# Performance work log

Hardware: AMD Instinct MI355X
Metric: run time of the kernel (lower is better)

Reference implementation:

```python
import jax, jax.numpy as jnp
import numpy as np
from math import factorial

# ---- static sizes from S2ConvNet_original ----
B_IN, B1, B2 = 30, 10, 6   # bandwidths: input S2 grid, after conv1 (SO3), after conv2 (SO3)
F1, F2, FOUT = 20, 40, 10
BATCH = 128


def _wigner_d(l, beta):
    """Wigner small-d matrix d^l_{m',m}(beta); rows m'=-l..l, cols m=-l..l."""
    cb, sb = np.cos(beta / 2.0), np.sin(beta / 2.0)
    d = np.zeros((2 * l + 1, 2 * l + 1))
    for i, mp in enumerate(range(-l, l + 1)):
        for j, m in enumerate(range(-l, l + 1)):
            pref = np.sqrt(float(factorial(l + mp) * factorial(l - mp) * factorial(l + m) * factorial(l - m)))
            acc = 0.0
            for s in range(max(0, m - mp), min(l + m, l - mp) + 1):
                den = factorial(l + m - s) * factorial(s) * factorial(mp - m + s) * factorial(l - mp - s)
                acc += ((-1.0) ** (mp - m + s) / den) * cb ** (2 * l + m - mp - 2 * s) * sb ** (mp - m + 2 * s)
            d[i, j] = pref * acc
    return d


def _dh_quad(b):
    """Driscoll-Healy beta grid / weights: sum_j w_j g(beta_j) ~ int_0^pi g(b) sin(b) db."""
    j = np.arange(2 * b)
    beta = np.pi * (2 * j + 1) / (4 * b)
    k = np.arange(b)[:, None]
    w = (2.0 / b) * np.sin(beta) * np.sum(np.sin((2 * k + 1) * beta[None, :]) / (2 * k + 1), axis=0)
    return beta, w


def _s2_grid(max_beta=np.pi / 8, n_alpha=8, n_beta=3):
    beta = np.arange(1, n_beta + 1) * max_beta / n_beta
    alpha = np.linspace(0, 2 * np.pi, n_alpha, endpoint=False)
    Bm, Am = np.meshgrid(beta, alpha, indexing='ij')
    return np.stack([Bm.ravel(), Am.ravel()], 1)  # [24, 2]


def _so3_grid(max_beta=np.pi / 8, max_gamma=2 * np.pi, n_alpha=8, n_beta=3, n_gamma=8):
    beta = np.arange(1, n_beta + 1) * max_beta / n_beta
    alpha = np.linspace(0, 2 * np.pi, n_alpha, endpoint=False)
    pre_gamma = np.linspace(0, max_gamma, n_gamma, endpoint=False)
    Bm, Am, Cm = np.meshgrid(beta, alpha, pre_gamma, indexing='ij')
    return np.stack([Bm.ravel(), Am.ravel(), (Cm - Am).ravel()], 1)  # [192, 3]


# ---------- conv1: S2 analysis (b 30 -> 10) ----------
_beta30, _qw30 = _dh_quad(B_IN)
_A1 = np.concatenate(
    [np.stack([_wigner_d(l, bb)[:, l] for bb in _beta30])  # d^l_{m,0}(beta_j): [60, 2l+1]
     * (_qw30 * (2 * np.pi / (2 * B_IN)))[:, None]
     for l in range(B1)], axis=1)  # [60, 100]
_A1J = jnp.asarray(_A1.astype(np.float32))
_M1 = np.concatenate([np.arange(-l, l + 1) for l in range(B1)])
_M1_IDX = np.mod(_M1, 2 * B_IN)

_g1 = _s2_grid()
_Y1 = np.concatenate(
    [np.stack([_wigner_d(l, bb)[:, l] for bb in _g1[:, 0]])
     * np.exp(-1j * np.outer(_g1[:, 1], np.arange(-l, l + 1)))
     for l in range(B1)], axis=1)  # [24, 100] complex
_Y1J = jnp.asarray(_Y1.astype(np.complex64))
_SC1 = float(1.0 / np.sqrt(len(_g1) * 1 * (B1 ** 4) / (B_IN ** 2)))

# ---------- SO3 synthesis tables at b=10 ----------
_beta10, _qw10 = _dh_quad(B1)
_D1S = [jnp.asarray(((2 * l + 1) * np.stack([_wigner_d(l, bb) for bb in _beta10])).astype(np.float32)) for l in range(B1)]
_FM1 = [np.mod(np.arange(-l, l + 1), 2 * B1) for l in range(B1)]

# ---------- conv2: SO3 analysis (b 10 -> 6) ----------
_W3 = np.concatenate(
    [(np.stack([_wigner_d(l, bb) for bb in _beta10])  # [20, 2l+1, 2l+1]
      * (_qw10 * (2 * np.pi / (2 * B1)) ** 2)[:, None, None]).reshape(2 * B1, -1)
     for l in range(B2)], axis=1)  # [20, 286]
_W3J = jnp.asarray(_W3.astype(np.float32))
_M2 = np.concatenate([np.repeat(np.arange(-l, l + 1), 2 * l + 1) for l in range(B2)])
_N2 = np.concatenate([np.tile(np.arange(-l, l + 1), 2 * l + 1) for l in range(B2)])
_M2_IDX = np.mod(_M2, 2 * B1)
_N2_IDX = np.mod(_N2, 2 * B1)

_g2 = _so3_grid()
_Y2 = np.concatenate(
    [np.stack([_wigner_d(l, bb) for bb in _g2[:, 0]]).reshape(len(_g2), -1)
     * (np.exp(-1j * np.outer(_g2[:, 1], np.arange(-l, l + 1)))[:, :, None]
        * np.exp(-1j * np.outer(_g2[:, 2], np.arange(-l, l + 1)))[:, None, :]).reshape(len(_g2), -1)
     for l in range(B2)], axis=1)  # [192, 286] complex: D^l_{mn}(alpha,beta,gamma)
_Y2J = jnp.asarray(_Y2.astype(np.complex64))
_SC2 = float(1.0 / np.sqrt(len(_g2) * F1 * (B2 ** 3) / (B1 ** 3)))

# ---------- SO3 synthesis tables at b=6 + integration weights ----------
_beta6, _qw6 = _dh_quad(B2)
_D2S = [jnp.asarray(((2 * l + 1) * np.stack([_wigner_d(l, bb) for bb in _beta6])).astype(np.float32)) for l in range(B2)]
_FM2 = [np.mod(np.arange(-l, l + 1), 2 * B2) for l in range(B2)]
_W_INT = jnp.asarray((_qw6 * (2 * np.pi / (2 * B2)) ** 2).astype(np.float32))


def _forward(x, k1, bias1, k2, bias2, w_out, b_lin):
    Bn = x.shape[0]
    # ===== conv1: S2 correlation -> function on SO(3) at b=10 =====
    xf = jnp.fft.fft(x.astype(jnp.complex64), axis=-1)                 # FFT over alpha: [B,1,60,60]
    xhat = jnp.einsum('bfjs,js->sbf', xf[..., _M1_IDX], _A1J)          # [100,B,1] S2 spectrum
    k1h = jnp.einsum('iop,ps->sio', (k1 * _SC1).astype(jnp.complex64), _Y1J)  # [100,1,F1]
    Ffreq = jnp.zeros((Bn, F1, 2 * B1, 2 * B1, 2 * B1), jnp.complex64)  # [B,F1,beta,m,n]
    for l in range(B1):
        s0, s1 = l * l, (l + 1) * (l + 1)
        # z^l_{mn} = sum_fin xhat^l_m conj(khat^l_n)  (outer product per degree l)
        zl = jnp.einsum('mbi,nio->bmno', xhat[s0:s1], jnp.conj(k1h[s0:s1]))
        fb = jnp.einsum('bmno,jmn->bojmn', zl, _D1S[l])                # (2l+1) d^l_{mn}(beta_j)
        Ffreq = Ffreq.at[:, :, :, _FM1[l][:, None], _FM1[l][None, :]].add(fb)
    x1 = jnp.fft.ifft2(Ffreq, axes=(-2, -1)).real * float((2 * B1) ** 2)  # synth over alpha,gamma
    x1 = jax.nn.relu(x1 + bias1[None, :, None, None, None])            # [B,F1,20,20,20]
    # ===== conv2: SO(3) correlation -> b=6 =====
    x1f = jnp.fft.fft2(x1.astype(jnp.complex64), axes=(-2, -1))        # FFT over alpha,gamma
    xhat2 = jnp.einsum('bfjs,js->sbf', x1f[:, :, :, _M2_IDX, _N2_IDX], _W3J)  # [286,B,F1]
    k2h = jnp.einsum('iop,ps->sio', (k2 * _SC2).astype(jnp.complex64), _Y2J)  # [286,F1,F2]
    Ffreq2 = jnp.zeros((Bn, F2, 2 * B2, 2 * B2, 2 * B2), jnp.complex64)
    base = 0
    for l in range(B2):
        L = 2 * l + 1
        xl = xhat2[base:base + L * L].reshape(L, L, Bn, F1)            # [m,k,B,Fin]
        gl = jnp.conj(k2h[base:base + L * L].reshape(L, L, F1, F2))    # [n,k,Fin,Fout]
        zl = jnp.einsum('mkbi,nkio->bmno', xl, gl)                     # z^l = xhat^l ghat^l^H
        fb = jnp.einsum('bmno,jmn->bojmn', zl, _D2S[l])
        Ffreq2 = Ffreq2.at[:, :, :, _FM2[l][:, None], _FM2[l][None, :]].add(fb)
        base += L * L
    x2 = jnp.fft.ifft2(Ffreq2, axes=(-2, -1)).real * float((2 * B2) ** 2)
    x2 = jax.nn.relu(x2 + bias2[None, :, None, None, None])            # [B,F2,12,12,12]
    # ===== so3_integrate + linear head =====
    feat = jnp.einsum('bfjkp,j->bf', x2, _W_INT)                       # [B,F2]
    return feat @ w_out.T + b_lin


def setup_inputs() -> dict:
    key = jax.random.key(0)
    ks = jax.random.split(key, 4)
    return {
        'x': jax.random.normal(ks[0], (BATCH, 1, 2 * B_IN, 2 * B_IN), jnp.float32),
        'k1': jax.random.normal(ks[1], (1, F1, len(_g1)), jnp.float32),
        'bias1': jnp.zeros((F1,), jnp.float32),
        'k2': jax.random.normal(ks[2], (F1, F2, len(_g2)), jnp.float32),
        'bias2': jnp.zeros((F2,), jnp.float32),
        'w_out': jax.random.normal(ks[3], (FOUT, F2), jnp.float32) / np.sqrt(F2).astype(np.float32),
        'b_lin': jnp.zeros((FOUT,), jnp.float32),
    }


def reference(x, k1, bias1, k2, bias2, w_out, b_lin):
    return _forward(x, k1, bias1, k2, bias2, w_out, b_lin)
```

## Files before the change

### kernel.cpp

```cpp
#include <hip/hip_runtime.h>
#include <math.h>

#define PI_D 3.14159265358979323846

#define BATCH 128
#define F1 20
#define F2 40
#define FOUT 10
#define NS1 100
#define NS2 286
#define NH2 146

typedef float v2f __attribute__((ext_vector_type(2)));
#define PKFMA(a,b,c) __builtin_elementwise_fma((a),(b),(c))
#define SW(v) __builtin_shufflevector((v),(v),1,0)
static __device__ __forceinline__ v2f bc2(float s){ return (v2f){s,s}; }
static __device__ __forceinline__ v2f ldv(const float2* p){ return *(const v2f*)p; }

#define GLOAD_LDS16(g,l) __builtin_amdgcn_global_load_lds( \
  (const __attribute__((address_space(1))) void*)(g), \
  (__attribute__((address_space(3))) void*)(l), 16, 0, 0)

__constant__ int ZB10c[11] = {0,1,10,35,84,165,286,455,680,969,1330};
__constant__ int B2OFFc[7] = {0,1,10,35,84,165,286};
__constant__ int HOFFc[7]  = {0,1,6,19,44,85,146};
__constant__ float2 E8c[8] = {
  { 1.f, 0.f}, { 0.70710678118654752f,-0.70710678118654752f},
  { 0.f,-1.f}, {-0.70710678118654752f,-0.70710678118654752f},
  {-1.f, 0.f}, {-0.70710678118654752f, 0.70710678118654752f},
  { 0.f, 1.f}, { 0.70710678118654752f, 0.70710678118654752f}};

#define WFENCE do{ __builtin_amdgcn_sched_barrier(0); \
  asm volatile("s_waitcnt lgkmcnt(0)" ::: "memory"); \
  __builtin_amdgcn_sched_barrier(0); }while(0)

__device__ inline void h_decode(int h, int& l, int& m, int& n){
  l=0; while(HOFFc[l+1]<=h) ++l;
  int r=h-HOFFc[l], L=2*l+1;
  if(r<l+1){ n=0; m=r; }
  else { int q=r-(l+1); n=q/L+1; m=q%L-l; }
}

__device__ inline double ipow_d(double x, int n){ double r=1.0; for(int i=0;i<n;++i) r*=x; return r; }
__device__ inline double dfact(int n){ double r=1.0; for(int i=2;i<=n;++i) r*=(double)i; return r; }

__device__ double wigd(int l, int mp, int m, double beta){
  double cb=cos(0.5*beta), sb=sin(0.5*beta);
  double pref=sqrt(dfact(l+mp)*dfact(l-mp)*dfact(l+m)*dfact(l-m));
  int s0 = (m-mp>0) ? (m-mp) : 0;
  int s1 = (l+m < l-mp) ? (l+m) : (l-mp);
  double acc=0.0;
  for(int s=s0;s<=s1;++s){
    double den=dfact(l+m-s)*dfact(s)*dfact(mp-m+s)*dfact(l-mp-s);
    double t=ipow_d(cb,2*l+m-mp-2*s)*ipow_d(sb,mp-m+2*s)/den;
    acc += ((mp-m+s)&1)? -t : t;
  }
  return pref*acc;
}

__device__ double dhw(int b, int j){
  double beta=PI_D*(2*j+1)/(4.0*b);
  double s=0.0;
  for(int k=0;k<b;++k) s += sin((2*k+1)*beta)/(2*k+1);
  return (2.0/b)*sin(beta)*s;
}

__device__ inline float2 cmulc(float2 a, float2 b){
  return make_float2(a.x*b.x + a.y*b.y, a.y*b.x - a.x*b.y);
}

__global__ void gen_all(float* A1, float* D1SJ, float* W3H, float* D2SJ,
                        float* D3_2, float* D3_1, float* WINT,
                        float2* E60, float2* E20, float2* E12,
                        unsigned* zLUT, unsigned* xh2LUT, unsigned* h2LUT,
                        unsigned short* fhLUT, unsigned* aLUT){
  __shared__ double dhwS[60];
  int blk=blockIdx.x, t=threadIdx.x;
  if(blk<24){
    if(t<60) dhwS[t]=dhw(30,t);
    __syncthreads();
    int idx=blk*256+t;
    if(idx<6000){
      int j=idx/NS1, s=idx%NS1;
      int l=0; while((l+1)*(l+1)<=s) ++l;
      int m=s-l*l-l;
      double beta=PI_D*(2*j+1)/120.0;
      A1[idx]=(float)(wigd(l,m,0,beta)*dhwS[j]*(2.0*PI_D/60.0));
    }
  } else if(blk<76){
    int idx=(blk-24)*256+t; if(idx>=13300) return;
    int j=idx/1330, s=idx%1330;
    int l=0; while(ZB10c[l+1]<=s) ++l;
    int r=s-ZB10c[l]; int L=2*l+1;
    int mi=r/L, ni=r%L;
    double beta=PI_D*(2*j+1)/40.0;
    float v=(float)((2*l+1)*wigd(l,mi-l,ni-l,beta));
    D1SJ[j*1330+s]=v;
    int s2=ZB10c[l]+(2*l-mi)*L+ni;
    D1SJ[(19-j)*1330+s2]=(ni&1)? -v : v;
  } else if(blk<82){
    if(t<20) dhwS[t]=dhw(10,t);
    __syncthreads();
    int idx=(blk-76)*256+t;
    if(idx<10*NH2){
      int j=idx/NH2, h=idx%NH2;
      int l,m,n; h_decode(h,l,m,n);
      double beta=PI_D*(2*j+1)/40.0;
      double c=2.0*PI_D/20.0;
      float v=(float)(wigd(l,m,n,beta)*dhwS[j]*c*c);
      W3H[j*NH2+h]=v;
      if(n==0){
        W3H[(19-j)*NH2+h]=((l+m)&1)? -v : v;
      } else {
        int L=2*l+1;
        int hp=HOFFc[l]+(l+1)+(n-1)*L+(l-m);
        W3H[(19-j)*NH2+hp]=((l+n)&1)? -v : v;
      }
    }
  } else if(blk<89){
    int idx=(blk-82)*256+t; if(idx>=1716) return;
    int j=idx/286, s=idx%286;
    int l=0; while(B2OFFc[l+1]<=s) ++l;
    int r=s-B2OFFc[l]; int L=2*l+1;
    int mi=r/L, ni=r%L;
    double beta=PI_D*(2*j+1)/24.0;
    float v=(float)((2*l+1)*wigd(l,mi-l,ni-l,beta));
    D2SJ[j*286+s]=v;
    int s2=B2OFFc[l]+(2*l-mi)*L+ni;
    D2SJ[(11-j)*286+s2]=(ni&1)? -v : v;
  } else if(blk<93){
    int idx=(blk-89)*256+t; if(idx>=3*286) return;
    int bi=idx/286, s=idx%286;
    int l=0; while(B2OFFc[l+1]<=s) ++l;
    int r=s-B2OFFc[l]; int L=2*l+1;
    int mi=r/L, ni=r%L;
    double beta=(bi+1)*(PI_D/8.0)/3.0;
    D3_2[idx]=(float)wigd(l,mi-l,ni-l,beta);
  } else if(blk<95){
    int idx=(blk-93)*256+t; if(idx>=3*100) return;
    int bi=idx/100, s=idx%100;
    int l=0; while((l+1)*(l+1)<=s) ++l;
    int m=s-l*l-l;
    double beta=(bi+1)*(PI_D/8.0)/3.0;
    D3_1[idx]=(float)wigd(l,m,0,beta);
  } else if(blk==95){
    if(t<12){ double c=2.0*PI_D/12.0; WINT[t]=(float)(dhw(6,t)*c*c); }
    if(t<60){ double a=2.0*PI_D*t/60.0; E60[t]=make_float2((float)cos(a),(float)sin(a)); }
    if(t<20){ double a=2.0*PI_D*t/20.0; E20[t]=make_float2((float)cos(a),(float)sin(a)); }
    if(t<12){ double a=2.0*PI_D*t/12.0; E12[t]=make_float2((float)cos(a),(float)sin(a)); }
  } else if(blk<102){
    int idx=(blk-96)*256+t; if(idx>=1330) return;
    int l=0; while(ZB10c[l+1]<=idx) ++l;
    int r=idx-ZB10c[l], L=2*l+1;
    int mi=r/L, ni=r%L;
    unsigned s1x=(unsigned)(l*l+mi), s1k=(unsigned)(l*l+ni);
    zLUT[idx]=s1x|(s1k<<16);
  } else if(blk==102){
    if(t<146){
      int l,m,n; h_decode(t,l,m,n);
      int L=2*l+1;
      int s2 =B2OFFc[l]+(m+l)*L+(n+l);
      int s2p=B2OFFc[l]+(l-m)*L+(l-n);
      unsigned sg=(unsigned)((m+n)&1);
      xh2LUT[t]=(unsigned)s2 | ((unsigned)s2p<<10) | (sg<<20);
      h2LUT[t]=(unsigned)l | ((unsigned)(m+l)<<4) | ((unsigned)(n+l)<<8) | ((unsigned)s2<<12);
      fhLUT[t]=(unsigned short)((n==0)? m : 6+(n-1)*11+(m+5));
    }
  } else {
    if(t==0){
      int idx=0;
      for(int lm=0;lm<10;++lm){
        for(int m=0;m<10;++m){
          int nlo=(m==0)?0:-9;
          for(int n=nlo;n<10;++n){
            int an=n<0?-n:n;
            int lmin=m>an?m:an;
            if(lmin!=lm) continue;
            int L=2*lm+1;
            int zi=ZB10c[lm]+(m+lm)*L+(n+lm);
            aLUT[idx++]=(unsigned)zi | ((unsigned)m<<11) | ((unsigned)(n+9)<<15) | ((unsigned)lm<<20);
          }
        }
      }
    }
  }
}

__global__ __launch_bounds__(256) void front_k(const float* __restrict__ x,
    const float* __restrict__ k1, const float* __restrict__ k2,
    const float2* __restrict__ E60, const float* __restrict__ A1,
    const float* __restrict__ D3_1,
    float2* __restrict__ XHAT, float2* __restrict__ K1H, float2* __restrict__ KA){
  __shared__ float2 E8s[8];
  int blk=blockIdx.x, t=threadIdx.x;
  if(blk<128){
    __shared__ __align__(16) float xs[3600];
    __shared__ float2 E60s[60];
    __shared__ float2 XFs[1140];
    if(t<60){ float2 e=E60[t]; E60s[t]=make_float2(e.x,-e.y); }
    {
      const float4* src=(const float4*)(x+blk*3600);
      float4* dst=(float4*)xs;
      for(int i=t;i<900;i+=256) GLOAD_LDS16(src+i, dst+(i&~63));
    }
    __syncthreads();
    for(int idx=t; idx<1140; idx+=256){
      int j=idx/19, mi=idx%19;
      int step=(mi<9)? mi+51 : mi-9;
      const float* xr=xs+j*60;
      v2f acc={0.f,0.f};
      int k=0;
      for(int a=0;a<60;++a){
        acc=PKFMA(bc2(xr[a]), ldv(&E60s[k]), acc);
        k+=step; if(k>=60)k-=60;
      }
      XFs[idx]=make_float2(acc.x,acc.y);
    }
    __syncthreads();
    for(int s=t; s<100; s+=256){
      int l=0; while((l+1)*(l+1)<=s) ++l;
      int m=s-l*l-l;
      const float2* xf=&XFs[m+9];
      v2f acc={0.f,0.f};
      for(int j=0;j<60;++j){
        acc=PKFMA(bc2(A1[j*NS1+s]), ldv(&xf[j*19]), acc);
      }
      XHAT[blk*NS1+s]=make_float2(acc.x,acc.y);
    }
  } else if(blk<136){
    if(t<8) E8s[t]=E8c[t];
    __syncthreads();
    int idx=(blk-128)*256+t;
    if(idx<F1*NS1){
      int o=idx/NS1, s=idx%NS1;
      int l=0; while((l+1)*(l+1)<=s) ++l;
      int m=s-l*l-l;
      int mm=m&7;
      v2f acc={0.f,0.f};
      for(int bi=0;bi<3;++bi){
        v2f sum={0.f,0.f};
        int q=0;
        #pragma unroll
        for(int ai=0;ai<8;++ai){
          sum=PKFMA(bc2(k1[o*24+bi*8+ai]), ldv(&E8s[q]), sum);
          q=(q+mm)&7;
        }
        acc=PKFMA(bc2(D3_1[bi*100+s]), sum, acc);
      }
      const float SC1f = 0.06123724356957945f;
      K1H[idx]=make_float2(acc.x*SC1f, acc.y*SC1f);
    }
  } else {
    if(t<8) E8s[t]=E8c[t];
    __syncthreads();
    int idx=(blk-136)*256+t;
    if(idx<153600){
      int ai=idx&7, q=(idx>>3)&7;
      int r2=idx>>6;
      int bi=r2%3, io=r2/3;
      const float* kp=k2+(size_t)io*192+bi*64+ai*8;
      v2f acc={0.f,0.f};
      int ph=0;
      #pragma unroll
      for(int gi=0;gi<8;++gi){
        acc=PKFMA(bc2(kp[gi]), ldv(&E8s[ph]), acc);
        ph=(ph+q)&7;
      }
      KA[(size_t)io*192+bi*64+q*8+ai]=make_float2(acc.x,acc.y);
    }
  }
}

__global__ __launch_bounds__(256,6) void fused1(
    const float2* __restrict__ XHAT, const float2* __restrict__ K1H,
    const float* __restrict__ D1SJ, const float* __restrict__ W3H,
    const float2* __restrict__ E20, const float* __restrict__ bias1,
    const unsigned* __restrict__ zLUT, const unsigned* __restrict__ xh2LUT,
    const unsigned short* __restrict__ fhLUT, const unsigned* __restrict__ aLUT,
    float2* __restrict__ XH2){
  const int b=blockIdx.x, o=blockIdx.y, t=threadIdx.x;
  const int ln=t&63, w=t>>6;
  __shared__ __align__(16) float2 zS[1330];
  __shared__ __align__(16) float2 TWE2[400];
  __shared__ __align__(16) float2 regA[4][200];
  __shared__ __align__(16) float2 regB[4][190];

  for(int idx=t; idx<400; idx+=256){
    int r=idx/20, c=idx%20;
    TWE2[idx]=E20[(r*c)%20];
  }
  {
    float2* st=regA[0];
    if(t<100) st[t]=XHAT[b*NS1+t];
    else if(t<200) st[t]=K1H[o*NS1+(t-100)];
  }
  __syncthreads();
  {
    const float2* st=regA[0];
    for(int idx=t; idx<1330; idx+=256){
      unsigned u=zLUT[idx];
      v2f xa=ldv(&st[u&0xffff]);
      v2f kb=ldv(&st[100+(u>>16)]);
      v2f p1=xa*kb, p2=xa*SW(kb);
      zS[idx]=make_float2(p1.x+p1.y, p2.y-p2.x);
    }
  }
  __syncthreads();

  const float bb1=bias1[o];
  float2* G  = regA[w];
  float*  vbF= (float*)regA[w];
  float2* Fq = regA[w];
  float*  RB = (float*)regB[w];
  float*  Sx = RB;
  float*  Sy = RB+180;
  float*  T0f= RB+360;
  float2* U_T= regB[w];
  v2f fa0={0.f,0.f}, fa1=fa0, fa2=fa0;

  const int BROW[19]={11,12,13,14,15,16,17,18,19,0,1,2,3,4,5,6,7,8,9};

  for(int jq=0;jq<5;++jq){
    const int j=jq*4+w;
    const float* Dg=D1SJ + j*1330;
    for(int idx=ln; idx<181; idx+=64){
      unsigned au=aLUT[idx];
      int zi=au&2047;
      int m=(au>>11)&15, n9=(au>>15)&31, l=(au>>20)&15;
      int L=2*l+1;
      int m2=2*m+2;
      v2f a0={0.f,0.f};
      for(; l<10; ++l){
        a0=PKFMA(ldv(&zS[zi]), bc2(Dg[zi]), a0);
        zi += L*L + 2*L + m2; L += 2;
      }
      *(v2f*)&G[m*19+n9]=a0;
    }
    WFENCE;
    if(ln<45){
      int mb=ln/5+1, gp=(ln%5)*2;
      const float2* Gr=&G[mb*19];
      v2f E1a={0.f,0.f},E2a=E1a,O1a=E1a,O2a=E1a;
      v2f E1b=E1a,E2b=E1a,O1b=E1a,O2b=E1a;
      #pragma unroll
      for(int c=0;c<19;++c){
        v2f gv=ldv(&Gr[c]);
        const float* er=(const float*)&TWE2[BROW[c]*20+gp];
        float4 e01=*(const float4*)er;
        v2f e0={e01.x,e01.y}, e1={e01.z,e01.w};
        if(c&1){
          E1a=PKFMA(gv,e0,E1a); E2a=PKFMA(gv,SW(e0),E2a);
          E1b=PKFMA(gv,e1,E1b); E2b=PKFMA(gv,SW(e1),E2b);
        } else {
          O1a=PKFMA(gv,e0,O1a); O2a=PKFMA(gv,SW(e0),O2a);
          O1b=PKFMA(gv,e1,O1b); O2b=PKFMA(gv,SW(e1),O2b);
        }
      }
      int si=(mb-1)*20+gp;
      float exa=E1a.x-E1a.y, oxa=O1a.x-O1a.y;
      float eya=E2a.x+E2a.y, oya=O2a.x+O2a.y;
      float exb=E1b.x-E1b.y, oxb=O1b.x-O1b.y;
      float eyb=E2b.x+E2b.y, oyb=O2b.x+O2b.y;
      *(v2f*)&Sx[si]   =(v2f){2.f*(exa+oxa), 2.f*(exb+oxb)};
      *(v2f*)&Sx[si+10]=(v2f){2.f*(exa-oxa), 2.f*(exb-oxb)};
      *(v2f*)&Sy[si]   =(v2f){2.f*(eya+oya), 2.f*(eyb+oyb)};
      *(v2f*)&Sy[si+10]=(v2f){2.f*(eya-oya), 2.f*(eyb-oyb)};
    } else if(ln<50){
      int gt=(ln-45)*2;
      float g0x=G[9].x;
      float Ea=0.f,Eb=0.f,Oa=0.f,Ob=0.f;
      #pragma unroll
      for(int n=1;n<10;++n){
        float2 gv=G[9+n];
        const float* er=(const float*)&TWE2[n*20+gt];
        float4 e01=*(const float4*)er;
        float ra=gv.x*e01.x-gv.y*e01.y;
        float rb=gv.x*e01.z-gv.y*e01.w;
        if((n&1)==0){ Ea+=ra; Eb+=rb; } else { Oa+=ra; Ob+=rb; }
      }
      T0f[gt]   =g0x+2.f*(Ea+Oa);
      T0f[gt+1] =g0x+2.f*(Eb+Ob);
      T0f[gt+10]=g0x+2.f*(Ea-Oa);
      T0f[gt+11]=g0x+2.f*(Eb-Ob);
    }
    WFENCE;
    if(ln<50){
      int a=ln/5, g0=(ln%5)*4;
      v2f i01={T0f[g0]+bb1, T0f[g0+1]+bb1};
      v2f i23={T0f[g0+2]+bb1, T0f[g0+3]+bb1};
      v2f P01={0.f,0.f},P23=P01,Q01=P01,Q23=P01;
      #pragma unroll
      for(int m=1;m<10;++m){
        float2 e=TWE2[a*20+m];
        v2f sx01=*(const v2f*)&Sx[(m-1)*20+g0];
        v2f sx23=*(const v2f*)&Sx[(m-1)*20+g0+2];
        v2f sy01=*(const v2f*)&Sy[(m-1)*20+g0];
        v2f sy23=*(const v2f*)&Sy[(m-1)*20+g0+2];
        if(m&1){
          Q01=PKFMA(bc2(e.x),sx01,Q01); Q01=PKFMA(bc2(-e.y),sy01,Q01);
          Q23=PKFMA(bc2(e.x),sx23,Q23); Q23=PKFMA(bc2(-e.y),sy23,Q23);
        } else {
          P01=PKFMA(bc2(e.x),sx01,P01); P01=PKFMA(bc2(-e.y),sy01,P01);
          P23=PKFMA(bc2(e.x),sx23,P23); P23=PKFMA(bc2(-e.y),sy23,P23);
        }
      }
      v2f z2={0.f,0.f};
      v2f vA01=i01+P01+Q01, vA23=i23+P23+Q23;
      v2f vB01=i01+P01-Q01, vB23=i23+P23-Q23;
      *(v2f*)&vbF[a*20+g0]       =__builtin_elementwise_max(vA01,z2);
      *(v2f*)&vbF[a*20+g0+2]     =__builtin_elementwise_max(vA23,z2);
      *(v2f*)&vbF[(a+10)*20+g0]  =__builtin_elementwise_max(vB01,z2);
      *(v2f*)&vbF[(a+10)*20+g0+2]=__builtin_elementwise_max(vB23,z2);
    }
    WFENCE;
    if(ln<60){
      int a=ln/3, np=ln%3;
      int nu0=2*np, nu1=2*np+1;
      int r0=(np==0)?0:(20-2*np);
      int r1=19-2*np;
      const float* vp=&vbF[a*20];
      const float2* T0r=&TWE2[r0*20];
      const float2* T1r=&TWE2[r1*20];
      v2f u0={0.f,0.f}, u1=u0;
      #pragma unroll
      for(int g=0;g<20;++g){
        v2f xb=bc2(vp[g]);
        u0=PKFMA(xb, ldv(&T0r[g]), u0);
        u1=PKFMA(xb, ldv(&T1r[g]), u1);
      }
      *(v2f*)&U_T[nu0*20+a]=u0; *(v2f*)&U_T[nu1*20+a]=u1;
    }
    WFENCE;
    if(ln<61){
      int mu,nu;
      if(ln<6){ mu=ln; nu=0; } else { int q=ln-6; nu=q/11+1; mu=q%11-5; }
      int mm=(mu+20)%20;
      int rm=(20-mm)%20;
      const float2* Ur=&U_T[nu*20];
      const float2* Er=&TWE2[rm*20];
      v2f p1={0.f,0.f}, p2=p1;
      #pragma unroll
      for(int a=0;a<20;++a){
        v2f u=ldv(&Ur[a]), e=ldv(&Er[a]);
        p1=PKFMA(u,e,p1);
        p2=PKFMA(u,SW(e),p2);
      }
      Fq[ln]=make_float2(p1.x-p1.y, p2.x+p2.y);
    }
    WFENCE;
    {
      const float* W3r=W3H + j*NH2;
      fa0=PKFMA(bc2(W3r[ln]),    ldv(&Fq[fhLUT[ln]]),    fa0);
      fa1=PKFMA(bc2(W3r[64+ln]), ldv(&Fq[fhLUT[64+ln]]), fa1);
      if(ln<18) fa2=PKFMA(bc2(W3r[128+ln]), ldv(&Fq[fhLUT[128+ln]]), fa2);
    }
    WFENCE;
  }
  regB[w][ln]=make_float2(fa0.x,fa0.y);
  regB[w][64+ln]=make_float2(fa1.x,fa1.y);
  if(ln<18) regB[w][128+ln]=make_float2(fa2.x,fa2.y);
  __syncthreads();
  for(int h=t; h<146; h+=256){
    unsigned u=xh2LUT[h];
    int s2=u&1023, s2p=(u>>10)&1023;
    float sg=((u>>20)&1)? -1.f : 1.f;
    float2 a0=regB[0][h], a1=regB[1][h], a2=regB[2][h], a3=regB[3][h];
    float2 a=make_float2(a0.x+a1.x+a2.x+a3.x, a0.y+a1.y+a2.y+a3.y);
    XH2[(b*286+s2 )*F1+o]=a;
    XH2[(b*286+s2p)*F1+o]=make_float2(sg*a.x, -sg*a.y);
  }
}

__global__ __launch_bounds__(192) void k2h_k(const float2* __restrict__ KA,
                      const float* __restrict__ D3_2,
                      const unsigned* __restrict__ h2LUT, const unsigned* __restrict__ xh2LUT,
                      float2* __restrict__ K2H){
  __shared__ float2 kaS[192];
  __shared__ float2 E8s[8];
  int io=blockIdx.x, t=threadIdx.x;
  int i=io/F2, o=io%F2;
  if(t<8) E8s[t]=E8c[t];
  kaS[t]=KA[(size_t)io*192+t];
  __syncthreads();
  if(t>=146) return;
  unsigned hu=h2LUT[t];
  int l=hu&15, mi=(hu>>4)&15, ni=(hu>>8)&15, s2=hu>>12;
  int m=mi-l, n=ni-l;
  unsigned xu=xh2LUT[t];
  int s2p=(xu>>10)&1023;
  float sg=((xu>>20)&1)? -1.f : 1.f;
  int q=n&7, p=(m-n)&7;
  v2f a1={0.f,0.f}, a2=a1;
  for(int bi=0;bi<3;++bi){
    const float2* kp=&kaS[bi*64+q*8];
    v2f s1={0.f,0.f}, s2v=s1;
    int ph=0;
    #pragma unroll
    for(int ai=0;ai<8;++ai){
      v2f ka=ldv(&kp[ai]), e=ldv(&E8s[ph]);
      s1=PKFMA(ka,e,s1); s2v=PKFMA(ka,SW(e),s2v);
      ph=(ph+p)&7;
    }
    v2f dv=bc2(D3_2[bi*286+s2]);
    a1=PKFMA(dv,s1,a1); a2=PKFMA(dv,s2v,a2);
  }
  const float SC2f = 0.034722222222222224f;
  float re=(a1.x-a1.y)*SC2f, im=(a2.x+a2.y)*SC2f;
  K2H[((size_t)o*286+s2)*F1+i]=make_float2(re,im);
  K2H[((size_t)o*286+s2p)*F1+i]=make_float2(sg*re,-sg*im);
}

__global__ __launch_bounds__(256,3) void fused2(
    const float2* __restrict__ XH2, const float2* __restrict__ K2H,
    const float* __restrict__ D2SJ, const float* __restrict__ WINT,
    const float2* __restrict__ E12, const float* __restrict__ bias2,
    const unsigned* __restrict__ h2LUT, const unsigned* __restrict__ xh2LUT,
    float* __restrict__ FEAT){
  const int b=blockIdx.x, o=blockIdx.y, t=threadIdx.x;
  const int ln=t&63, w=t>>6;
  __shared__ __align__(16) float2 Xs[2420];
  __shared__ __align__(16) float2 Ks[2420];
  __shared__ float2 zpS[1144];
  __shared__ float2 z2S[286];
  __shared__ float  redS[256];
  float2* alias=(float2*)Xs;
  float2* TWE12=alias;

  const int gb[4]={0,84,165,286};
  const int hb[4]={0,44,85,146};
  for(int grp=0; grp<3; ++grp){
    int row0=gb[grp], rows=gb[grp+1]-row0;
    {
      int cnt4=rows*10;
      const float4* xsrc=(const float4*)(XH2+(size_t)(b*286+row0)*F1);
      const float4* ksrc=(const float4*)(K2H+(size_t)(o*286+row0)*F1);
      float4* xd=(float4*)Xs; float4* kd=(float4*)Ks;
      for(int i4=t;i4<cnt4;i4+=256){
        int wb=i4&~63;
        GLOAD_LDS16(xsrc+i4, xd+wb);
        GLOAD_LDS16(ksrc+i4, kd+wb);
      }
    }
    __syncthreads();
    int nh=hb[grp+1]-hb[grp];
    for(int idx=t; idx<4*nh; idx+=256){
      int hl=idx>>2, iq=idx&3;
      int h=hb[grp]+hl;
      unsigned hu=h2LUT[h];
      int l=hu&15, mi=(hu>>4)&15, ni=(hu>>8)&15, s2=hu>>12;
      int L=2*l+1;
      int xr0=(B2OFFc[l]-row0)+mi*L;
      int kr0=(B2OFFc[l]-row0)+ni*L;
      v2f p1={0.f,0.f}, p2=p1;
      for(int k=0;k<L;++k){
        const float2* xp=Xs+(xr0+k)*F1+iq*5;
        const float2* kp=Ks+(kr0+k)*F1+iq*5;
        #pragma unroll
        for(int i=0;i<5;++i){
          v2f xa=ldv(&xp[i]), kb=ldv(&kp[i]);
          p1=PKFMA(xa,kb,p1);
          p2=PKFMA(xa,SW(kb),p2);
        }
      }
      zpS[iq*286+s2]=make_float2(p1.x+p1.y, p2.y-p2.x);
    }
    __syncthreads();
  }
  for(int idx=t; idx<146; idx+=256){
    unsigned xu=xh2LUT[idx];
    int s2=xu&1023, s2p=(xu>>10)&1023;
    float sg=((xu>>20)&1)? -1.f : 1.f;
    float2 a;
    a.x=zpS[0*286+s2].x+zpS[1*286+s2].x+zpS[2*286+s2].x+zpS[3*286+s2].x;
    a.y=zpS[0*286+s2].y+zpS[1*286+s2].y+zpS[2*286+s2].y+zpS[3*286+s2].y;
    z2S[s2]=a;
    z2S[s2p]=make_float2(sg*a.x,-sg*a.y);
  }
  __syncthreads();
  for(int idx=t; idx<144; idx+=256){
    int r=idx/12, c=idx%12;
    TWE12[idx]=E12[(r*c)%12];
  }
  __syncthreads();

  float2* base2=alias+144+w*400;
  float2* G2_0=base2; float2* G2_1=base2+66; float2* G2_2=base2+132;
  float*  SP=(float*)(base2+198);
  float*  S2x0=SP, *S2x1=SP+60, *S2x2=SP+120;
  float*  S2y0=SP+180, *S2y1=SP+240, *S2y2=SP+300;
  float*  T02=SP+360;
  float personal=0.f;
  const float b2v=bias2[o];
  const int j0=3*w, j1=3*w+1, j2=3*w+2;
  const float* Dg0=D2SJ + j0*286;
  const float* Dg1=D2SJ + j1*286;
  const float* Dg2=D2SJ + j2*286;
  const int BR12[11]={7,8,9,10,11,0,1,2,3,4,5};

  if(ln<61){
    int m,n;
    if(ln<6){m=0;n=ln;} else {int qq=ln-6;m=qq/11+1;n=qq%11-5;}
    int an=n<0?-n:n; int l=m>an?m:an; int L=2*l+1;
    int zi=B2OFFc[l]+(m+l)*L+(n+l); int m2=2*m+2;
    v2f a0={0.f,0.f}, a1=a0, a2=a0;
    for(;l<6;++l){
      v2f zv=ldv(&z2S[zi]);
      a0=PKFMA(zv, bc2(Dg0[zi]), a0);
      a1=PKFMA(zv, bc2(Dg1[zi]), a1);
      a2=PKFMA(zv, bc2(Dg2[zi]), a2);
      zi+=L*L+2*L+m2; L+=2;
    }
    int gi=m*11+(n+5);
    *(v2f*)&G2_0[gi]=a0; *(v2f*)&G2_1[gi]=a1; *(v2f*)&G2_2[gi]=a2;
  }
  WFENCE;
  if(ln<30){
    int m=ln/6+1, g=(ln%6)*2;
    v2f p10={0.f,0.f},p20=p10,p11=p10,p21=p10;
    v2f q10=p10,q20=p10,q11=p10,q21=p10;
    v2f r10=p10,r20=p10,r11=p10,r21=p10;
    #pragma unroll
    for(int c=0;c<11;++c){
      float4 eq=*(const float4*)&TWE12[BR12[c]*12+g];
      v2f e0={eq.x,eq.y}, e1={eq.z,eq.w};
      v2f g0=ldv(&G2_0[m*11+c]), g1=ldv(&G2_1[m*11+c]), g2=ldv(&G2_2[m*11+c]);
      p10=PKFMA(g0,e0,p10); p20=PKFMA(g0,SW(e0),p20);
      p11=PKFMA(g0,e1,p11); p21=PKFMA(g0,SW(e1),p21);
      q10=PKFMA(g1,e0,q10); q20=PKFMA(g1,SW(e0),q20);
      q11=PKFMA(g1,e1,q11); q21=PKFMA(g1,SW(e1),q21);
      r10=PKFMA(g2,e0,r10); r20=PKFMA(g2,SW(e0),r20);
      r11=PKFMA(g2,e1,r11); r21=PKFMA(g2,SW(e1),r21);
    }
    int si=(m-1)*12+g;
    S2x0[si]=2.f*(p10.x-p10.y); S2x0[si+1]=2.f*(p11.x-p11.y);
    S2y0[si]=2.f*(p20.x+p20.y); S2y0[si+1]=2.f*(p21.x+p21.y);
    S2x1[si]=2.f*(q10.x-q10.y); S2x1[si+1]=2.f*(q11.x-q11.y);
    S2y1[si]=2.f*(q20.x+q20.y); S2y1[si+1]=2.f*(q21.x+q21.y);
    S2x2[si]=2.f*(r10.x-r10.y); S2x2[si+1]=2.f*(r11.x-r11.y);
    S2y2[si]=2.f*(r20.x+r20.y); S2y2[si+1]=2.f*(r21.x+r21.y);
  } else if(ln<42){
    int g=ln-30;
    float r0=G2_0[5].x, r1=G2_1[5].x, r2=G2_2[5].x;
    #pragma unroll
    for(int n=1;n<6;++n){
      float2 e=TWE12[n*12+g];
      float2 g0=G2_0[5+n], g1=G2_1[5+n], g2=G2_2[5+n];
      r0+=2.f*(g0.x*e.x-g0.y*e.y);
      r1+=2.f*(g1.x*e.x-g1.y*e.y);
      r2+=2.f*(g2.x*e.x-g2.y*e.y);
    }
    T02[g]=r0; T02[12+g]=r1; T02[24+g]=r2;
  }
  WFENCE;
  if(ln<36){
    float w0=WINT[j0], w1=WINT[j1], w2=WINT[j2];
    int a=ln/3, g4=(ln%3)*4;
    v2f iA0={T02[g4]+b2v, T02[g4+1]+b2v},       iB0={T02[g4+2]+b2v, T02[g4+3]+b2v};
    v2f iA1={T02[12+g4]+b2v, T02[12+g4+1]+b2v}, iB1={T02[12+g4+2]+b2v, T02[12+g4+3]+b2v};
    v2f iA2={T02[24+g4]+b2v, T02[24+g4+1]+b2v}, iB2={T02[24+g4+2]+b2v, T02[24+g4+3]+b2v};
    #pragma unroll
    for(int m=1;m<6;++m){
      float2 e=TWE12[a*12+m];
      v2f ex=bc2(e.x), eny=bc2(-e.y);
      int si=(m-1)*12+g4;
      v2f sx, sy;
      sx=*(const v2f*)&S2x0[si];   sy=*(const v2f*)&S2y0[si];
      iA0=PKFMA(ex,sx,iA0); iA0=PKFMA(eny,sy,iA0);
      sx=*(const v2f*)&S2x0[si+2]; sy=*(const v2f*)&S2y0[si+2];
      iB0=PKFMA(ex,sx,iB0); iB0=PKFMA(eny,sy,iB0);
      sx=*(const v2f*)&S2x1[si];   sy=*(const v2f*)&S2y1[si];
      iA1=PKFMA(ex,sx,iA1); iA1=PKFMA(eny,sy,iA1);
      sx=*(const v2f*)&S2x1[si+2]; sy=*(const v2f*)&S2y1[si+2];
      iB1=PKFMA(ex,sx,iB1); iB1=PKFMA(eny,sy,iB1);
      sx=*(const v2f*)&S2x2[si];   sy=*(const v2f*)&S2y2[si];
      iA2=PKFMA(ex,sx,iA2); iA2=PKFMA(eny,sy,iA2);
      sx=*(const v2f*)&S2x2[si+2]; sy=*(const v2f*)&S2y2[si+2];
      iB2=PKFMA(ex,sx,iB2); iB2=PKFMA(eny,sy,iB2);
    }
    v2f z2={0.f,0.f};
    v2f rA0=__builtin_elementwise_max(iA0,z2), rB0=__builtin_elementwise_max(iB0,z2);
    v2f rA1=__builtin_elementwise_max(iA1,z2), rB1=__builtin_elementwise_max(iB1,z2);
    v2f rA2=__builtin_elementwise_max(iA2,z2), rB2=__builtin_elementwise_max(iB2,z2);
    personal += w0*(rA0.x+rA0.y+rB0.x+rB0.y)
              + w1*(rA1.x+rA1.y+rB1.x+rB1.y)
              + w2*(rA2.x+rA2.y+rB2.x+rB2.y);
  }
  redS[t]=personal;
  __syncthreads();
  for(int s=128;s>0;s>>=1){
    if(t<s) redS[t]+=redS[t+s];
    __syncthreads();
  }
  if(t==0) FEAT[b*F2+o]=redS[0];
}

__global__ void head_k(const float* __restrict__ FEAT, const float* __restrict__ w_out,
                       const float* __restrict__ b_lin, float* __restrict__ out){
  int idx=blockIdx.x*blockDim.x+threadIdx.x;
  if(idx>=BATCH*FOUT) return;
  int b=idx/FOUT, q=idx%FOUT;
  float acc=b_lin[q];
  for(int f=0;f<F2;++f) acc += FEAT[b*F2+f]*w_out[q*F2+f];
  out[idx]=acc;
}

extern "C" void kernel_launch(void* const* d_in, const int* in_sizes, int n_in,
                              void* d_out, int out_size, void* d_ws, size_t ws_size,
                              hipStream_t stream) {
  const float* x    =(const float*)d_in[0];
  const float* k1   =(const float*)d_in[1];
  const float* bias1=(const float*)d_in[2];
  const float* k2   =(const float*)d_in[3];
  const float* bias2=(const float*)d_in[4];
  const float* w_out=(const float*)d_in[5];
  const float* b_lin=(const float*)d_in[6];
  float* out=(float*)d_out;

  char* ws=(char*)d_ws;
  float*  A1   =(float* )(ws+0);
  float*  D1SJ =(float* )(ws+24000);
  float*  W3H  =(float* )(ws+130400);
  float*  D2SJ =(float* )(ws+142080);
  float*  D3_2 =(float* )(ws+155808);
  float*  D3_1 =(float* )(ws+159248);
  float*  WINT =(float* )(ws+160448);
  float2* E60  =(float2*)(ws+160496);
  float2* E20  =(float2*)(ws+160976);
  float2* E12  =(float2*)(ws+161136);
  unsigned* zLUT=(unsigned*)(ws+161248);
  unsigned* xh2LUT=(unsigned*)(ws+166576);
  unsigned* h2LUT =(unsigned*)(ws+167160);
  unsigned short* fhLUT=(unsigned short*)(ws+167744);
  unsigned* aLUT =(unsigned*)(ws+168048);
  float2* XHAT =(float2*)(ws+168784);
  float2* K1H  =(float2*)(ws+271184);
  float2* KA   =(float2*)(ws+287184);
  float2* XH2  =(float2*)(ws+1515984);
  float2* K2H  =(float2*)(ws+7373264);
  float*  FEAT =(float* )(ws+9203664);

  (void)in_sizes; (void)n_in; (void)out_size; (void)ws_size;

  gen_all<<<104,256,0,stream>>>(A1,D1SJ,W3H,D2SJ,D3_2,D3_1,WINT,E60,E20,E12,
                                zLUT,xh2LUT,h2LUT,fhLUT,aLUT);
  front_k<<<736,256,0,stream>>>(x,k1,k2,E60,A1,D3_1,XHAT,K1H,KA);
  dim3 g1(BATCH,F1);
  fused1<<<g1,256,0,stream>>>(XHAT,K1H,D1SJ,W3H,E20,bias1,zLUT,xh2LUT,fhLUT,aLUT,XH2);
  k2h_k<<<F1*F2,192,0,stream>>>(KA,D3_2,h2LUT,xh2LUT,K2H);
  dim3 g2(BATCH,F2);
  fused2<<<g2,256,0,stream>>>(XH2,K2H,D2SJ,WINT,E12,bias2,h2LUT,xh2LUT,FEAT);
  head_k<<<(BATCH*FOUT+255)/256,256,0,stream>>>(FEAT,w_out,b_lin,out);
}
```

Baseline: 218.0 us.

## Fold DFT half-periods and widen fused1 to eight waves per block

The front-end alpha DFT and two inverse-DFT stages in fused1 now combine x[a] and x[a+N/2] with a sign set by frequency parity, which halves the multiply-accumulate loop lengths. fused1 also moves from 4 to 8 waves per block, so the 20 beta slices are covered in 3 rounds instead of 5. The third round leaves 4 of 8 waves idle. The larger LDS arrays and 512-thread blocks may reduce how many blocks fit on a CU.

```diff
diff --git a/kernel.cpp b/kernel.cpp
--- a/kernel.cpp
+++ b/kernel.cpp
@@ -207,11 +207,13 @@
     for(int idx=t; idx<1140; idx+=256){
       int j=idx/19, mi=idx%19;
       int step=(mi<9)? mi+51 : mi-9;
+      bool modd = ((mi&1)==0);
       const float* xr=xs+j*60;
       v2f acc={0.f,0.f};
       int k=0;
-      for(int a=0;a<60;++a){
-        acc=PKFMA(bc2(xr[a]), ldv(&E60s[k]), acc);
+      for(int a=0;a<30;++a){
+        float xv = modd ? (xr[a]-xr[a+30]) : (xr[a]+xr[a+30]);
+        acc=PKFMA(bc2(xv), ldv(&E60s[k]), acc);
         k+=step; if(k>=60)k-=60;
       }
       XFs[idx]=make_float2(acc.x,acc.y);
@@ -271,7 +273,7 @@
   }
 }
 
-__global__ __launch_bounds__(256,6) void fused1(
+__global__ __launch_bounds__(512,6) void fused1(
     const float2* __restrict__ XHAT, const float2* __restrict__ K1H,
     const float* __restrict__ D1SJ, const float* __restrict__ W3H,
     const float2* __restrict__ E20, const float* __restrict__ bias1,
@@ -282,10 +284,10 @@
   const int ln=t&63, w=t>>6;
   __shared__ __align__(16) float2 zS[1330];
   __shared__ __align__(16) float2 TWE2[400];
-  __shared__ __align__(16) float2 regA[4][200];
-  __shared__ __align__(16) float2 regB[4][190];
-
-  for(int idx=t; idx<400; idx+=256){
+  __shared__ __align__(16) float2 regA[8][200];
+  __shared__ __align__(16) float2 regB[8][190];
+
+  for(int idx=t; idx<400; idx+=512){
     int r=idx/20, c=idx%20;
     TWE2[idx]=E20[(r*c)%20];
   }
@@ -297,7 +299,7 @@
   __syncthreads();
   {
     const float2* st=regA[0];
-    for(int idx=t; idx<1330; idx+=256){
+    for(int idx=t; idx<1330; idx+=512){
       unsigned u=zLUT[idx];
       v2f xa=ldv(&st[u&0xffff]);
       v2f kb=ldv(&st[100+(u>>16)]);
@@ -320,10 +322,11 @@
 
   const int BROW[19]={11,12,13,14,15,16,17,18,19,0,1,2,3,4,5,6,7,8,9};
 
-  for(int jq=0;jq<5;++jq){
-    const int j=jq*4+w;
-    const float* Dg=D1SJ + j*1330;
-    for(int idx=ln; idx<181; idx+=64){
+  for(int jq=0;jq<3;++jq){
+    const int j=jq*8+w;
+    const bool act=(j<20);
+    const float* Dg=D1SJ + (act? j*1330 : 0);
+    if(act) for(int idx=ln; idx<181; idx+=64){
       unsigned au=aLUT[idx];
       int zi=au&2047;
       int m=(au>>11)&15, n9=(au>>15)&31, l=(au>>20)&15;
@@ -337,6 +340,7 @@
       *(v2f*)&G[m*19+n9]=a0;
     }
     WFENCE;
+    if(act){
     if(ln<45){
       int mb=ln/5+1, gp=(ln%5)*2;
       const float2* Gr=&G[mb*19];
@@ -383,8 +387,9 @@
       T0f[gt+10]=g0x+2.f*(Ea-Oa);
       T0f[gt+11]=g0x+2.f*(Eb-Ob);
     }
+    }
     WFENCE;
-    if(ln<50){
+    if(act && ln<50){
       int a=ln/5, g0=(ln%5)*4;
       v2f i01={T0f[g0]+bb1, T0f[g0+1]+bb1};
       v2f i23={T0f[g0+2]+bb1, T0f[g0+3]+bb1};
@@ -413,7 +418,7 @@
       *(v2f*)&vbF[(a+10)*20+g0+2]=__builtin_elementwise_max(vB23,z2);
     }
     WFENCE;
-    if(ln<60){
+    if(act && ln<60){
       int a=ln/3, np=ln%3;
       int nu0=2*np, nu1=2*np+1;
       int r0=(np==0)?0:(20-2*np);
@@ -423,32 +428,35 @@
       const float2* T1r=&TWE2[r1*20];
       v2f u0={0.f,0.f}, u1=u0;
       #pragma unroll
-      for(int g=0;g<20;++g){
-        v2f xb=bc2(vp[g]);
-        u0=PKFMA(xb, ldv(&T0r[g]), u0);
-        u1=PKFMA(xb, ldv(&T1r[g]), u1);
+      for(int g=0;g<10;++g){
+        float va=vp[g], vb=vp[g+10];
+        u0=PKFMA(bc2(va+vb), ldv(&T0r[g]), u0);
+        u1=PKFMA(bc2(va-vb), ldv(&T1r[g]), u1);
       }
       *(v2f*)&U_T[nu0*20+a]=u0; *(v2f*)&U_T[nu1*20+a]=u1;
     }
     WFENCE;
-    if(ln<61){
+    if(act && ln<61){
       int mu,nu;
       if(ln<6){ mu=ln; nu=0; } else { int q=ln-6; nu=q/11+1; mu=q%11-5; }
       int mm=(mu+20)%20;
       int rm=(20-mm)%20;
+      bool modd=(mm&1);
       const float2* Ur=&U_T[nu*20];
       const float2* Er=&TWE2[rm*20];
       v2f p1={0.f,0.f}, p2=p1;
       #pragma unroll
-      for(int a=0;a<20;++a){
-        v2f u=ldv(&Ur[a]), e=ldv(&Er[a]);
+      for(int a=0;a<10;++a){
+        v2f ua=ldv(&Ur[a]), ub=ldv(&Ur[a+10]);
+        v2f u = modd ? (ua-ub) : (ua+ub);
+        v2f e=ldv(&Er[a]);
         p1=PKFMA(u,e,p1);
         p2=PKFMA(u,SW(e),p2);
       }
       Fq[ln]=make_float2(p1.x-p1.y, p2.x+p2.y);
     }
     WFENCE;
-    {
+    if(act){
       const float* W3r=W3H + j*NH2;
       fa0=PKFMA(bc2(W3r[ln]),    ldv(&Fq[fhLUT[ln]]),    fa0);
       fa1=PKFMA(bc2(W3r[64+ln]), ldv(&Fq[fhLUT[64+ln]]), fa1);
@@ -460,12 +468,14 @@
   regB[w][64+ln]=make_float2(fa1.x,fa1.y);
   if(ln<18) regB[w][128+ln]=make_float2(fa2.x,fa2.y);
   __syncthreads();
-  for(int h=t; h<146; h+=256){
+  for(int h=t; h<146; h+=512){
     unsigned u=xh2LUT[h];
     int s2=u&1023, s2p=(u>>10)&1023;
     float sg=((u>>20)&1)? -1.f : 1.f;
     float2 a0=regB[0][h], a1=regB[1][h], a2=regB[2][h], a3=regB[3][h];
-    float2 a=make_float2(a0.x+a1.x+a2.x+a3.x, a0.y+a1.y+a2.y+a3.y);
+    float2 a4=regB[4][h], a5=regB[5][h], a6=regB[6][h], a7=regB[7][h];
+    float2 a=make_float2(a0.x+a1.x+a2.x+a3.x+a4.x+a5.x+a6.x+a7.x,
+                         a0.y+a1.y+a2.y+a3.y+a4.y+a5.y+a6.y+a7.y);
     XH2[(b*286+s2 )*F1+o]=a;
     XH2[(b*286+s2p)*F1+o]=make_float2(sg*a.x, -sg*a.y);
   }
@@ -745,7 +755,7 @@
                                 zLUT,xh2LUT,h2LUT,fhLUT,aLUT);
   front_k<<<736,256,0,stream>>>(x,k1,k2,E60,A1,D3_1,XHAT,K1H,KA);
   dim3 g1(BATCH,F1);
-  fused1<<<g1,256,0,stream>>>(XHAT,K1H,D1SJ,W3H,E20,bias1,zLUT,xh2LUT,fhLUT,aLUT,XH2);
+  fused1<<<g1,512,0,stream>>>(XHAT,K1H,D1SJ,W3H,E20,bias1,zLUT,xh2LUT,fhLUT,aLUT,XH2);
   k2h_k<<<F1*F2,192,0,stream>>>(KA,D3_2,h2LUT,xh2LUT,K2H);
   dim3 g2(BATCH,F2);
   fused2<<<g2,256,0,stream>>>(XH2,K2H,D2SJ,WINT,E12,bias2,h2LUT,xh2LUT,FEAT);
```

New measurement: 212.8 us. -2.4%, faster.
